# Kernel optimization log

Hardware: AMD Instinct MI355X
Metric: run time of the kernel (lower is better)

## Reference

```python
import jax, jax.numpy as jnp
import numpy as np

ALPHA = 0.2          # LeakyReLU negative slope
NEG_INF = -9e15      # matches torch's -9000000000000000.0 mask value


def _gat_layer(x, adj_mask, W, a1, a2, concat):
    """One GraphAttentionLayerBatch (eval mode, dropout off).

    The original builds a_input = [h_i || h_j] of shape [B,N,N,2F] and dots
    with a = [a1; a2]; that is mathematically the separable score
    a1.h_i + a2.h_j, which we compute directly without the O(N^2*2F) tensor.
    """
    h = jnp.einsum('bnf,fo->bno', x, W)            # [B, N, F_out]
    f1 = jnp.einsum('bno,o->bn', h, a1)            # a1 . h_i
    f2 = jnp.einsum('bno,o->bn', h, a2)            # a2 . h_j
    e = jax.nn.leaky_relu(f1[:, :, None] + f2[:, None, :], negative_slope=ALPHA)
    e = jnp.where(adj_mask, e, NEG_INF)            # [B, N, N]
    att = jax.nn.softmax(e, axis=2)
    h_prime = jnp.einsum('bnm,bmo->bno', att, h)   # [B, N, F_out]
    return jax.nn.elu(h_prime) if concat else h_prime


def setup_inputs() -> dict:
    key = jax.random.key(0)
    ks = jax.random.split(key, 9)
    B, N, nfeat, nhid, nclass, H = 32, 512, 128, 64, 16, 8
    x = jax.random.normal(ks[0], (B, N, nfeat), dtype=jnp.float32)
    adj = jax.random.randint(ks[1], (B, N, N), 0, 2, dtype=jnp.int32)
    W_heads = jax.random.normal(ks[2], (H, nfeat, nhid), dtype=jnp.float32) * 0.1
    a1_heads = jax.random.normal(ks[3], (H, nhid), dtype=jnp.float32) * 0.1
    a2_heads = jax.random.normal(ks[4], (H, nhid), dtype=jnp.float32) * 0.1
    W_out = jax.random.normal(ks[5], (nhid * H, nclass), dtype=jnp.float32) * 0.05
    a1_out = jax.random.normal(ks[6], (nclass,), dtype=jnp.float32) * 0.1
    a2_out = jax.random.normal(ks[7], (nclass,), dtype=jnp.float32) * 0.1
    return {"x": x, "adj": adj, "W_heads": W_heads, "a1_heads": a1_heads,
            "a2_heads": a2_heads, "W_out": W_out, "a1_out": a1_out,
            "a2_out": a2_out}


def reference(x, adj, W_heads, a1_heads, a2_heads, W_out, a1_out, a2_out):
    mask = adj > 0  # [B, N, N]
    # multi-head attention layers (concat=True)
    heads = jax.vmap(lambda W, a1, a2: _gat_layer(x, mask, W, a1, a2, True))(
        W_heads, a1_heads, a2_heads)              # [H, B, N, nhid]
    H, B, N, F = heads.shape
    x_cat = jnp.transpose(heads, (1, 2, 0, 3)).reshape(B, N, H * F)
    # output attention layer (concat=False)
    return _gat_layer(x_cat, mask, W_out, a1_out, a2_out, False)
```

## Files before the change

kernel.cpp:

```cpp
#include <hip/hip_runtime.h>
#include <hip/hip_bf16.h>

#define GB 32
#define GN 512
#define GFIN 128
#define GFH 64
#define GH 8
#define GC 16

typedef short short8 __attribute__((ext_vector_type(8)));
typedef float f32x4 __attribute__((ext_vector_type(4)));

__device__ __forceinline__ ushort f2bf(float f) {
  unsigned u = __float_as_uint(f);
  return (ushort)((u + 0x7FFFu + ((u >> 16) & 1u)) >> 16);
}
__device__ __forceinline__ unsigned pk2(float a, float b) {
  float2 f2; f2.x = a; f2.y = b;
  __hip_bfloat162 h = __float22bfloat162_rn(f2);
  union { __hip_bfloat162 h; unsigned u; } cv;
  cv.h = h;
  return cv.u;
}
__device__ __forceinline__ short8 ones8() {
  short8 o;
#pragma unroll
  for (int i = 0; i < 8; ++i) o[i] = (short)0x3F80;
  return o;
}

__global__ __launch_bounds__(256) void k_pack_gemm1(
    const int* __restrict__ adj, unsigned* __restrict__ mw,
    const float* __restrict__ xg, const float* __restrict__ Wg,
    const float* __restrict__ a1g, const float* __restrict__ a2g,
    ushort* __restrict__ VTg, float* __restrict__ f1g, float* __restrict__ f2g,
    const float* __restrict__ Wog, ushort* __restrict__ WoT) {
  __shared__ ushort Wt[64][136];
  __shared__ ushort xl[128][136];
  int blk = blockIdx.x;
  int tid = threadIdx.x;

  if (blk == 5120) {
    for (int i = tid; i < 512 * GC; i += 256) {
      int k = i & 511, cc = i >> 9;
      WoT[cc * 512 + k] = f2bf(Wog[(size_t)k * GC + cc]);
    }
    return;
  }
  if (blk >= 1024) {
    int pblk = blk - 1024;
    int lane = tid & 63;
    int base = pblk * 2048 + tid;
    int v[8];
#pragma unroll
    for (int it = 0; it < 8; ++it) v[it] = adj[(size_t)base + it * 256];
#pragma unroll
    for (int it = 0; it < 8; ++it) {
      unsigned long long m = __ballot(v[it] > 0);
      int idx = base + it * 256;
      if (lane == 0)       mw[idx >> 5] = (unsigned)m;
      else if (lane == 32) mw[idx >> 5] = (unsigned)(m >> 32);
    }
    return;
  }

  int bh = blk >> 2, rq = blk & 3;
  int b = bh >> 3, h = bh & 7;
  int r0 = rq * 128;
  int lane = tid & 63, w = tid >> 6;
  int c = lane & 15, q = lane >> 4;

  const float* Wh = Wg + (size_t)h * GFIN * GFH;
  for (int i = tid; i < GFIN * GFH; i += 256) {
    int f = i >> 6, j = i & 63;
    Wt[j][f] = f2bf(Wh[i]);
  }
  const float* xb = xg + ((size_t)b * GN + r0) * GFIN;
  for (int u = tid; u < 128 * 32; u += 256) {
    int row = u >> 5, c4 = u & 31;
    float4 xf = *(const float4*)&xb[(size_t)row * GFIN + c4 * 4];
    uint2 us;
    us.x = pk2(xf.x, xf.y);
    us.y = pk2(xf.z, xf.w);
    *(uint2*)&xl[row][c4 * 4] = us;
  }
  __syncthreads();

  short8 Bf[4][4];
#pragma unroll
  for (int cb = 0; cb < 4; ++cb)
#pragma unroll
    for (int kk = 0; kk < 4; ++kk)
      Bf[cb][kk] = *(const short8*)&Wt[cb * 16 + c][kk * 32 + q * 8];

  float a1v[4], a2v[4];
#pragma unroll
  for (int cb = 0; cb < 4; ++cb) {
    a1v[cb] = a1g[h * 64 + cb * 16 + c];
    a2v[cb] = a2g[h * 64 + cb * 16 + c];
  }

  f32x4 acc[2][4];
#pragma unroll
  for (int r = 0; r < 2; ++r)
#pragma unroll
    for (int cb = 0; cb < 4; ++cb) acc[r][cb] = (f32x4){0.f, 0.f, 0.f, 0.f};

#pragma unroll
  for (int kk = 0; kk < 4; ++kk) {
    short8 A0 = *(const short8*)&xl[(w * 2 + 0) * 16 + c][kk * 32 + q * 8];
    short8 A1 = *(const short8*)&xl[(w * 2 + 1) * 16 + c][kk * 32 + q * 8];
#pragma unroll
    for (int cb = 0; cb < 4; ++cb) {
      acc[0][cb] = __builtin_amdgcn_mfma_f32_16x16x32_bf16(A0, Bf[cb][kk], acc[0][cb], 0, 0, 0);
      acc[1][cb] = __builtin_amdgcn_mfma_f32_16x16x32_bf16(A1, Bf[cb][kk], acc[1][cb], 0, 0, 0);
    }
  }

  ushort* VT = VTg + (size_t)bh * GN * GFH;
  float* f1o = f1g + (size_t)bh * GN;
  float* f2o = f2g + (size_t)bh * GN;
#pragma unroll
  for (int rbi = 0; rbi < 2; ++rbi) {
    int rowb = r0 + (w * 2 + rbi) * 16 + q * 4;
    float v1[4] = {0.f, 0.f, 0.f, 0.f}, v2[4] = {0.f, 0.f, 0.f, 0.f};
#pragma unroll
    for (int cb = 0; cb < 4; ++cb) {
      f32x4 a = acc[rbi][cb];
      uint2 vs;
      vs.x = pk2(a[0], a[1]);
      vs.y = pk2(a[2], a[3]);
      *(uint2*)&VT[(size_t)(cb * 16 + c) * GN + rowb] = vs;
#pragma unroll
      for (int i = 0; i < 4; ++i) {
        v1[i] += a[i] * a1v[cb];
        v2[i] += a[i] * a2v[cb];
      }
    }
#pragma unroll
    for (int i = 0; i < 4; ++i) {
#pragma unroll
      for (int off = 1; off < 16; off <<= 1) {
        v1[i] += __shfl_xor(v1[i], off);
        v2[i] += __shfl_xor(v2[i], off);
      }
      if (c == 0) { f1o[rowb + i] = v1[i]; f2o[rowb + i] = v2[i]; }
    }
  }
}

__global__ __launch_bounds__(256, 2) void k_attn1(
    const ushort* __restrict__ VTg, const unsigned* __restrict__ mwg,
    const float* __restrict__ f1g, const float* __restrict__ f2g,
    ushort* __restrict__ xcb) {
  __shared__ ushort P[2][32][520];
  int blk = blockIdx.x;
  int bh = blk & 255, rq = blk >> 8;
  int b = bh >> 3, h = bh & 7;
  int r0 = rq * 128;
  int tid = threadIdx.x, lane = tid & 63, w = tid >> 6;
  int c = lane & 15, q = lane >> 4;

  const unsigned* mwb = mwg + (size_t)b * GN * 16;
  const float* f1w = f1g + (size_t)bh * GN;
  const float* f2w = f2g + (size_t)bh * GN;

  float4 fa = *(const float4*)&f2w[lane * 8];
  float4 fb = *(const float4*)&f2w[lane * 8 + 4];
  float E2[8], e2[8];
  {
    float f2v[8] = {fa.x, fa.y, fa.z, fa.w, fb.x, fb.y, fb.z, fb.w};
#pragma unroll
    for (int i = 0; i < 8; ++i) {
      E2[i] = __expf(f2v[i]);
      e2[i] = __expf(0.2f * f2v[i]);
    }
  }
  float f1v = 0.f;
  if (lane < 32) f1v = f1w[r0 + ((lane >> 3) << 5) + w + ((lane & 7) << 2)];
  float E1v = __expf(f1v), e1v = __expf(0.2f * f1v);

  const ushort* VT = VTg + (size_t)bh * GN * GFH + (size_t)(w * 16 + c) * GN + q * 8;
  short8 Bf[16];
#pragma unroll
  for (int kk = 0; kk < 16; ++kk) Bf[kk] = *(const short8*)&VT[kk * 32];
  const short8 ONES = ones8();

  unsigned mn[8];
#pragma unroll
  for (int ri = 0; ri < 8; ++ri)
    mn[ri] = mwb[(size_t)(r0 + w + 4 * ri) * 16 + (lane >> 2)];
#pragma unroll
  for (int ri = 0; ri < 8; ++ri) {
    float E1r = __shfl(E1v, ri);
    float e1r = __shfl(e1v, ri);
    unsigned mb = (mn[ri] >> (8 * (lane & 3))) & 0xffu;
    float p[8];
#pragma unroll
    for (int i = 0; i < 8; ++i) {
      float v = fmaxf(E1r * E2[i], e1r * e2[i]);
      p[i] = ((mb >> i) & 1u) ? v : 0.f;
    }
    uint4 u;
    u.x = pk2(p[0], p[1]);
    u.y = pk2(p[2], p[3]);
    u.z = pk2(p[4], p[5]);
    u.w = pk2(p[6], p[7]);
    *(uint4*)&P[0][w + 4 * ri][lane * 8] = u;
  }
#pragma unroll
  for (int ri = 0; ri < 8; ++ri)
    mn[ri] = mwb[(size_t)(r0 + 32 + w + 4 * ri) * 16 + (lane >> 2)];
  __syncthreads();

#pragma unroll
  for (int t = 0; t < 4; ++t) {
    int tb = r0 + t * 32;
    const ushort (*Pc)[520] = P[t & 1];

    f32x4 acc0 = (f32x4){0.f, 0.f, 0.f, 0.f};
    f32x4 acc1 = (f32x4){0.f, 0.f, 0.f, 0.f};
    f32x4 aL0 = (f32x4){0.f, 0.f, 0.f, 0.f};
    f32x4 aL1 = (f32x4){0.f, 0.f, 0.f, 0.f};
#pragma unroll
    for (int kk = 0; kk < 16; ++kk) {
      short8 A0 = *(const short8*)&Pc[c][kk * 32 + q * 8];
      short8 A1 = *(const short8*)&Pc[16 + c][kk * 32 + q * 8];
      acc0 = __builtin_amdgcn_mfma_f32_16x16x32_bf16(A0, Bf[kk], acc0, 0, 0, 0);
      aL0  = __builtin_amdgcn_mfma_f32_16x16x32_bf16(A0, ONES,   aL0, 0, 0, 0);
      acc1 = __builtin_amdgcn_mfma_f32_16x16x32_bf16(A1, Bf[kk], acc1, 0, 0, 0);
      aL1  = __builtin_amdgcn_mfma_f32_16x16x32_bf16(A1, ONES,   aL1, 0, 0, 0);
    }

    if (t < 3) {
#pragma unroll
      for (int ri = 0; ri < 8; ++ri) {
        float E1r = __shfl(E1v, (t + 1) * 8 + ri);
        float e1r = __shfl(e1v, (t + 1) * 8 + ri);
        unsigned mb = (mn[ri] >> (8 * (lane & 3))) & 0xffu;
        float p[8];
#pragma unroll
        for (int i = 0; i < 8; ++i) {
          float v = fmaxf(E1r * E2[i], e1r * e2[i]);
          p[i] = ((mb >> i) & 1u) ? v : 0.f;
        }
        uint4 u;
        u.x = pk2(p[0], p[1]);
        u.y = pk2(p[2], p[3]);
        u.z = pk2(p[4], p[5]);
        u.w = pk2(p[6], p[7]);
        *(uint4*)&P[(t + 1) & 1][w + 4 * ri][lane * 8] = u;
      }
      if (t < 2) {
#pragma unroll
        for (int ri = 0; ri < 8; ++ri)
          mn[ri] = mwb[(size_t)(tb + 64 + w + 4 * ri) * 16 + (lane >> 2)];
      }
    }

#pragma unroll
    for (int rbi = 0; rbi < 2; ++rbi) {
      f32x4 a = rbi ? acc1 : acc0;
      f32x4 aL = rbi ? aL1 : aL0;
#pragma unroll
      for (int i = 0; i < 4; ++i) {
        int row = tb + rbi * 16 + q * 4 + i;
        float v = a[i] / fmaxf(aL[i], 1e-30f);
        v = v > 0.f ? v : __expf(v) - 1.f;
        xcb[((size_t)(b * GN + row)) * 512 + h * 64 + w * 16 + c] = f2bf(v);
      }
    }
    __syncthreads();
  }
}

__global__ __launch_bounds__(256) void k_gemm2(
    const ushort* __restrict__ xcb, const ushort* __restrict__ WoT,
    const float* __restrict__ a1o, const float* __restrict__ a2o,
    ushort* __restrict__ hTg, float* __restrict__ f1bg,
    float* __restrict__ f2bg) {
  int vb = blockIdx.x;
  int b = vb >> 3, r0 = (vb & 7) * 64;
  int tid = threadIdx.x, lane = tid & 63, w = tid >> 6;
  int c = lane & 15, q = lane >> 4;

  short8 Bf[16];
#pragma unroll
  for (int kk = 0; kk < 16; ++kk)
    Bf[kk] = *(const short8*)&WoT[(size_t)c * 512 + kk * 32 + q * 8];

  const ushort* xrow = xcb + ((size_t)(b * GN + r0 + w * 16 + c)) * 512 + q * 8;
  f32x4 acc = (f32x4){0.f, 0.f, 0.f, 0.f};
#pragma unroll
  for (int kk = 0; kk < 16; ++kk) {
    short8 A = *(const short8*)&xrow[kk * 32];
    acc = __builtin_amdgcn_mfma_f32_16x16x32_bf16(A, Bf[kk], acc, 0, 0, 0);
  }

  float a1v = a1o[c], a2v = a2o[c];
  int rowb = r0 + w * 16 + q * 4;
  uint2 vs;
  vs.x = pk2(acc[0], acc[1]);
  vs.y = pk2(acc[2], acc[3]);
  *(uint2*)&hTg[((size_t)b * GC + c) * 512 + rowb] = vs;
#pragma unroll
  for (int i = 0; i < 4; ++i) {
    float v1 = acc[i] * a1v, v2 = acc[i] * a2v;
#pragma unroll
    for (int off = 1; off < 16; off <<= 1) {
      v1 += __shfl_xor(v1, off);
      v2 += __shfl_xor(v2, off);
    }
    if (c == 0) {
      f1bg[(size_t)b * GN + rowb + i] = v1;
      f2bg[(size_t)b * GN + rowb + i] = v2;
    }
  }
}

__global__ __launch_bounds__(256) void k_attn2(
    const ushort* __restrict__ hTg, const unsigned* __restrict__ mwg,
    const float* __restrict__ f1g, const float* __restrict__ f2g,
    float* __restrict__ outg) {
  __shared__ ushort P[32][520];
  int vb = blockIdx.x;
  int b = vb >> 4, r0 = (vb & 15) * 32;
  int tid = threadIdx.x, lane = tid & 63, w = tid >> 6;
  int c = lane & 15, q = lane >> 4;
  const short8 ONES = ones8();

  const unsigned* mwb = mwg + (size_t)b * GN * 16;
  const float* f1w = f1g + (size_t)b * GN;
  const float* f2w = f2g + (size_t)b * GN;

  float4 fa = *(const float4*)&f2w[lane * 8];
  float4 fb = *(const float4*)&f2w[lane * 8 + 4];
  float E2[8], e2[8];
  {
    float f2v[8] = {fa.x, fa.y, fa.z, fa.w, fb.x, fb.y, fb.z, fb.w};
#pragma unroll
    for (int i = 0; i < 8; ++i) {
      E2[i] = __expf(f2v[i]);
      e2[i] = __expf(0.2f * f2v[i]);
    }
  }
  float f1v = 0.f;
  if (lane < 8) f1v = f1w[r0 + w * 8 + lane];
  float E1v = __expf(f1v), e1v = __expf(0.2f * f1v);

  unsigned mword[8];
#pragma unroll
  for (int ri = 0; ri < 8; ++ri)
    mword[ri] = mwb[(size_t)(r0 + w * 8 + ri) * 16 + (lane >> 2)];
#pragma unroll
  for (int ri = 0; ri < 8; ++ri) {
    float E1r = __shfl(E1v, ri);
    float e1r = __shfl(e1v, ri);
    unsigned mb = (mword[ri] >> (8 * (lane & 3))) & 0xffu;
    float p[8];
#pragma unroll
    for (int i = 0; i < 8; ++i) {
      float v = fmaxf(E1r * E2[i], e1r * e2[i]);
      p[i] = ((mb >> i) & 1u) ? v : 0.f;
    }
    uint4 u;
    u.x = pk2(p[0], p[1]);
    u.y = pk2(p[2], p[3]);
    u.z = pk2(p[4], p[5]);
    u.w = pk2(p[6], p[7]);
    *(uint4*)&P[w * 8 + ri][lane * 8] = u;
  }
  __syncthreads();

  if (w < 2) {
    short8 Bf[16];
#pragma unroll
    for (int kk = 0; kk < 16; ++kk)
      Bf[kk] = *(const short8*)&hTg[((size_t)b * GC + c) * 512 + kk * 32 + q * 8];
    f32x4 acc = (f32x4){0.f, 0.f, 0.f, 0.f};
    f32x4 aL = (f32x4){0.f, 0.f, 0.f, 0.f};
#pragma unroll
    for (int kk = 0; kk < 16; ++kk) {
      short8 A = *(const short8*)&P[w * 16 + c][kk * 32 + q * 8];
      acc = __builtin_amdgcn_mfma_f32_16x16x32_bf16(A, Bf[kk], acc, 0, 0, 0);
      aL  = __builtin_amdgcn_mfma_f32_16x16x32_bf16(A, ONES, aL, 0, 0, 0);
    }
#pragma unroll
    for (int i = 0; i < 4; ++i) {
      int row = r0 + w * 16 + q * 4 + i;
      outg[((size_t)(b * GN + row)) * GC + c] = acc[i] / fmaxf(aL[i], 1e-30f);
    }
  }
}

extern "C" void kernel_launch(void* const* d_in, const int* in_sizes, int n_in,
                              void* d_out, int out_size, void* d_ws, size_t ws_size,
                              hipStream_t stream) {
  (void)in_sizes; (void)n_in; (void)out_size;
  const float* x   = (const float*)d_in[0];
  const int*   adj = (const int*)d_in[1];
  const float* Whd = (const float*)d_in[2];
  const float* a1h = (const float*)d_in[3];
  const float* a2h = (const float*)d_in[4];
  const float* Wo  = (const float*)d_in[5];
  const float* a1o = (const float*)d_in[6];
  const float* a2o = (const float*)d_in[7];

  size_t off = 0;
  char* base = (char*)d_ws;
  unsigned* mw = (unsigned*)(base + off); off += (size_t)GB * GN * 16 * 4;
  ushort* VT   = (ushort*)(base + off);   off += (size_t)GB * GH * GN * GFH * 2;
  ushort* xcb  = (ushort*)(base + off);   off += (size_t)GB * GN * 512 * 2;
  ushort* WoT  = (ushort*)(base + off);   off += (size_t)GC * 512 * 2;
  ushort* hT   = (ushort*)(base + off);   off += (size_t)GB * GC * GN * 2;
  float* f1    = (float*)(base + off);    off += (size_t)GB * GH * GN * 4;
  float* f2    = (float*)(base + off);    off += (size_t)GB * GH * GN * 4;
  float* f1b   = (float*)(base + off);    off += (size_t)GB * GN * 4;
  float* f2b   = (float*)(base + off);    off += (size_t)GB * GN * 4;

  if (ws_size < off) return;

  hipLaunchKernelGGL(k_pack_gemm1, dim3(5121), dim3(256), 0, stream,
                     adj, mw, x, Whd, a1h, a2h, VT, f1, f2, Wo, WoT);
  hipLaunchKernelGGL(k_attn1, dim3(1024), dim3(256), 0, stream,
                     VT, mw, f1, f2, xcb);
  hipLaunchKernelGGL(k_gemm2, dim3(256), dim3(256), 0, stream,
                     xcb, WoT, a1o, a2o, hT, f1b, f2b);
  hipLaunchKernelGGL(k_attn2, dim3(512), dim3(256), 0, stream,
                     hT, mw, f1b, f2b, (float*)d_out);
}
```

Before: 155.2 us.

## Normalize softmax rows before matmul and split adjacency packing into separate kernel

Each attention row's denominator is now computed with a wave-wide shuffle reduction and the probabilities are scaled by its inverse before being packed to bf16. This drops the extra MFMA against a ones vector and the division in the epilogue, halving the matrix work in both attention kernels. Adjacency bit-packing moves out of the fused gemm1 launch into its own kernel that handles 16 elements per thread. The trade is six shuffle steps per row, and an extra launch with different overlap between packing and gemm1.

```diff
diff --git a/kernel.cpp b/kernel.cpp
--- a/kernel.cpp
+++ b/kernel.cpp
@@ -29,8 +29,23 @@
   return o;
 }
 
-__global__ __launch_bounds__(256) void k_pack_gemm1(
-    const int* __restrict__ adj, unsigned* __restrict__ mw,
+__global__ __launch_bounds__(256) void k_pack(const int* __restrict__ adj,
+                                              unsigned* __restrict__ mw) {
+  int tid = threadIdx.x, lane = tid & 63;
+  int base = blockIdx.x * 4096 + tid;
+  int v[16];
+#pragma unroll
+  for (int it = 0; it < 16; ++it) v[it] = adj[(size_t)base + it * 256];
+#pragma unroll
+  for (int it = 0; it < 16; ++it) {
+    unsigned long long m = __ballot(v[it] > 0);
+    int idx = base + it * 256;
+    if (lane == 0)       mw[idx >> 5] = (unsigned)m;
+    else if (lane == 32) mw[idx >> 5] = (unsigned)(m >> 32);
+  }
+}
+
+__global__ __launch_bounds__(256) void k_gemm1(
     const float* __restrict__ xg, const float* __restrict__ Wg,
     const float* __restrict__ a1g, const float* __restrict__ a2g,
     ushort* __restrict__ VTg, float* __restrict__ f1g, float* __restrict__ f2g,
@@ -40,26 +55,10 @@
   int blk = blockIdx.x;
   int tid = threadIdx.x;
 
-  if (blk == 5120) {
+  if (blk == 1024) {
     for (int i = tid; i < 512 * GC; i += 256) {
       int k = i & 511, cc = i >> 9;
       WoT[cc * 512 + k] = f2bf(Wog[(size_t)k * GC + cc]);
-    }
-    return;
-  }
-  if (blk >= 1024) {
-    int pblk = blk - 1024;
-    int lane = tid & 63;
-    int base = pblk * 2048 + tid;
-    int v[8];
-#pragma unroll
-    for (int it = 0; it < 8; ++it) v[it] = adj[(size_t)base + it * 256];
-#pragma unroll
-    for (int it = 0; it < 8; ++it) {
-      unsigned long long m = __ballot(v[it] > 0);
-      int idx = base + it * 256;
-      if (lane == 0)       mw[idx >> 5] = (unsigned)m;
-      else if (lane == 32) mw[idx >> 5] = (unsigned)(m >> 32);
     }
     return;
   }
@@ -184,7 +183,6 @@
   short8 Bf[16];
 #pragma unroll
   for (int kk = 0; kk < 16; ++kk) Bf[kk] = *(const short8*)&VT[kk * 32];
-  const short8 ONES = ones8();
 
   unsigned mn[8];
 #pragma unroll
@@ -195,17 +193,21 @@
     float E1r = __shfl(E1v, ri);
     float e1r = __shfl(e1v, ri);
     unsigned mb = (mn[ri] >> (8 * (lane & 3))) & 0xffu;
-    float p[8];
+    float p[8], L;
 #pragma unroll
     for (int i = 0; i < 8; ++i) {
       float v = fmaxf(E1r * E2[i], e1r * e2[i]);
       p[i] = ((mb >> i) & 1u) ? v : 0.f;
     }
+    L = ((p[0] + p[1]) + (p[2] + p[3])) + ((p[4] + p[5]) + (p[6] + p[7]));
+#pragma unroll
+    for (int off = 1; off < 64; off <<= 1) L += __shfl_xor(L, off);
+    float inv = 1.f / fmaxf(L, 1e-30f);
     uint4 u;
-    u.x = pk2(p[0], p[1]);
-    u.y = pk2(p[2], p[3]);
-    u.z = pk2(p[4], p[5]);
-    u.w = pk2(p[6], p[7]);
+    u.x = pk2(p[0] * inv, p[1] * inv);
+    u.y = pk2(p[2] * inv, p[3] * inv);
+    u.z = pk2(p[4] * inv, p[5] * inv);
+    u.w = pk2(p[6] * inv, p[7] * inv);
     *(uint4*)&P[0][w + 4 * ri][lane * 8] = u;
   }
 #pragma unroll
@@ -220,16 +222,12 @@
 
     f32x4 acc0 = (f32x4){0.f, 0.f, 0.f, 0.f};
     f32x4 acc1 = (f32x4){0.f, 0.f, 0.f, 0.f};
-    f32x4 aL0 = (f32x4){0.f, 0.f, 0.f, 0.f};
-    f32x4 aL1 = (f32x4){0.f, 0.f, 0.f, 0.f};
 #pragma unroll
     for (int kk = 0; kk < 16; ++kk) {
       short8 A0 = *(const short8*)&Pc[c][kk * 32 + q * 8];
       short8 A1 = *(const short8*)&Pc[16 + c][kk * 32 + q * 8];
       acc0 = __builtin_amdgcn_mfma_f32_16x16x32_bf16(A0, Bf[kk], acc0, 0, 0, 0);
-      aL0  = __builtin_amdgcn_mfma_f32_16x16x32_bf16(A0, ONES,   aL0, 0, 0, 0);
       acc1 = __builtin_amdgcn_mfma_f32_16x16x32_bf16(A1, Bf[kk], acc1, 0, 0, 0);
-      aL1  = __builtin_amdgcn_mfma_f32_16x16x32_bf16(A1, ONES,   aL1, 0, 0, 0);
     }
 
     if (t < 3) {
@@ -238,17 +236,21 @@
         float E1r = __shfl(E1v, (t + 1) * 8 + ri);
         float e1r = __shfl(e1v, (t + 1) * 8 + ri);
         unsigned mb = (mn[ri] >> (8 * (lane & 3))) & 0xffu;
-        float p[8];
+        float p[8], L;
 #pragma unroll
         for (int i = 0; i < 8; ++i) {
           float v = fmaxf(E1r * E2[i], e1r * e2[i]);
           p[i] = ((mb >> i) & 1u) ? v : 0.f;
         }
+        L = ((p[0] + p[1]) + (p[2] + p[3])) + ((p[4] + p[5]) + (p[6] + p[7]));
+#pragma unroll
+        for (int off = 1; off < 64; off <<= 1) L += __shfl_xor(L, off);
+        float inv = 1.f / fmaxf(L, 1e-30f);
         uint4 u;
-        u.x = pk2(p[0], p[1]);
-        u.y = pk2(p[2], p[3]);
-        u.z = pk2(p[4], p[5]);
-        u.w = pk2(p[6], p[7]);
+        u.x = pk2(p[0] * inv, p[1] * inv);
+        u.y = pk2(p[2] * inv, p[3] * inv);
+        u.z = pk2(p[4] * inv, p[5] * inv);
+        u.w = pk2(p[6] * inv, p[7] * inv);
         *(uint4*)&P[(t + 1) & 1][w + 4 * ri][lane * 8] = u;
       }
       if (t < 2) {
@@ -261,11 +263,10 @@
 #pragma unroll
     for (int rbi = 0; rbi < 2; ++rbi) {
       f32x4 a = rbi ? acc1 : acc0;
-      f32x4 aL = rbi ? aL1 : aL0;
 #pragma unroll
       for (int i = 0; i < 4; ++i) {
         int row = tb + rbi * 16 + q * 4 + i;
-        float v = a[i] / fmaxf(aL[i], 1e-30f);
+        float v = a[i];
         v = v > 0.f ? v : __expf(v) - 1.f;
         xcb[((size_t)(b * GN + row)) * 512 + h * 64 + w * 16 + c] = f2bf(v);
       }
@@ -327,7 +328,6 @@
   int b = vb >> 4, r0 = (vb & 15) * 32;
   int tid = threadIdx.x, lane = tid & 63, w = tid >> 6;
   int c = lane & 15, q = lane >> 4;
-  const short8 ONES = ones8();
 
   const unsigned* mwb = mwg + (size_t)b * GN * 16;
   const float* f1w = f1g + (size_t)b * GN;
@@ -357,17 +357,21 @@
     float E1r = __shfl(E1v, ri);
     float e1r = __shfl(e1v, ri);
     unsigned mb = (mword[ri] >> (8 * (lane & 3))) & 0xffu;
-    float p[8];
+    float p[8], L;
 #pragma unroll
     for (int i = 0; i < 8; ++i) {
       float v = fmaxf(E1r * E2[i], e1r * e2[i]);
       p[i] = ((mb >> i) & 1u) ? v : 0.f;
     }
+    L = ((p[0] + p[1]) + (p[2] + p[3])) + ((p[4] + p[5]) + (p[6] + p[7]));
+#pragma unroll
+    for (int off = 1; off < 64; off <<= 1) L += __shfl_xor(L, off);
+    float inv = 1.f / fmaxf(L, 1e-30f);
     uint4 u;
-    u.x = pk2(p[0], p[1]);
-    u.y = pk2(p[2], p[3]);
-    u.z = pk2(p[4], p[5]);
-    u.w = pk2(p[6], p[7]);
+    u.x = pk2(p[0] * inv, p[1] * inv);
+    u.y = pk2(p[2] * inv, p[3] * inv);
+    u.z = pk2(p[4] * inv, p[5] * inv);
+    u.w = pk2(p[6] * inv, p[7] * inv);
     *(uint4*)&P[w * 8 + ri][lane * 8] = u;
   }
   __syncthreads();
@@ -378,17 +382,15 @@
     for (int kk = 0; kk < 16; ++kk)
       Bf[kk] = *(const short8*)&hTg[((size_t)b * GC + c) * 512 + kk * 32 + q * 8];
     f32x4 acc = (f32x4){0.f, 0.f, 0.f, 0.f};
-    f32x4 aL = (f32x4){0.f, 0.f, 0.f, 0.f};
 #pragma unroll
     for (int kk = 0; kk < 16; ++kk) {
       short8 A = *(const short8*)&P[w * 16 + c][kk * 32 + q * 8];
       acc = __builtin_amdgcn_mfma_f32_16x16x32_bf16(A, Bf[kk], acc, 0, 0, 0);
-      aL  = __builtin_amdgcn_mfma_f32_16x16x32_bf16(A, ONES, aL, 0, 0, 0);
     }
 #pragma unroll
     for (int i = 0; i < 4; ++i) {
       int row = r0 + w * 16 + q * 4 + i;
-      outg[((size_t)(b * GN + row)) * GC + c] = acc[i] / fmaxf(aL[i], 1e-30f);
+      outg[((size_t)(b * GN + row)) * GC + c] = acc[i];
     }
   }
 }
@@ -420,8 +422,9 @@
 
   if (ws_size < off) return;
 
-  hipLaunchKernelGGL(k_pack_gemm1, dim3(5121), dim3(256), 0, stream,
-                     adj, mw, x, Whd, a1h, a2h, VT, f1, f2, Wo, WoT);
+  hipLaunchKernelGGL(k_pack, dim3(2048), dim3(256), 0, stream, adj, mw);
+  hipLaunchKernelGGL(k_gemm1, dim3(1025), dim3(256), 0, stream,
+                     x, Whd, a1h, a2h, VT, f1, f2, Wo, WoT);
   hipLaunchKernelGGL(k_attn1, dim3(1024), dim3(256), 0, stream,
                      VT, mw, f1, f2, xcb);
   hipLaunchKernelGGL(k_gemm2, dim3(256), dim3(256), 0, stream,
```

Result: slower. 165.5 us (+6.6%).
